# Optimization experiments

Hardware: AMD Instinct MI355X
Metric: run time of the kernel (lower is better)

## Reference

```python
import jax, jax.numpy as jnp
import numpy as np

N = 40000
E = 640000
IN_FEATS = 128
OUT_FEATS = 64
K = 8
FACTOR_DIM = OUT_FEATS // K  # 8
ITERATIONS = 3
TAU = 1.0
LEAKY_SLOPE = 0.01  # torch nn.LeakyReLU default


def setup_inputs() -> dict:
    key = jax.random.key(0)
    k1, k2, k3 = jax.random.split(key, 3)
    x = jax.random.normal(k1, (N, IN_FEATS), dtype=jnp.float32)
    # xavier_normal_ with gain=1.414: std = gain * sqrt(2 / (fan_in + fan_out))
    std = 1.414 * np.sqrt(2.0 / (IN_FEATS + OUT_FEATS))
    weight = jax.random.normal(k2, (IN_FEATS, OUT_FEATS), dtype=jnp.float32) * std
    bias = jnp.zeros((OUT_FEATS,), dtype=jnp.float32)
    edge_index = jax.random.randint(k3, (2, E), 0, N, dtype=jnp.int32)
    return {"x": x, "weight": weight, "bias": bias, "edge_index": edge_index}


def _l2norm(h):
    # h / ||h||_2 along last dim (no eps, matching torch code)
    return h / jnp.sqrt((h * h).sum(-1, keepdims=True))


def reference(x, weight, bias, edge_index):
    num_nodes = x.shape[0]
    src = edge_index[0]  # scatter target / softmax segment node
    dst = edge_index[1]  # gathered neighbor node

    h = jax.nn.leaky_relu(x @ weight + bias, LEAKY_SLOPE)          # [N, out]
    # split into K factors of FACTOR_DIM: [N, K, d]
    h = h.reshape(num_nodes, K, FACTOR_DIM)
    h_normed = _l2norm(h)                                           # [N, K, d]

    h_src = h_normed
    h_dst = h_normed
    for _ in range(ITERATIONS):
        feat_nbr = h_src[dst]                                       # [E, K, d]
        s = (h_dst[src] * feat_nbr).sum(-1) / TAU                   # [E, K]
        # segment softmax over edges grouped by src node
        smax = jax.ops.segment_max(s, src, num_segments=num_nodes)  # [N, K]
        ex = jnp.exp(s - smax[src])                                 # [E, K]
        denom = jax.ops.segment_sum(ex, src, num_segments=num_nodes)
        alpha = ex / denom[src]                                     # [E, K]
        msg = feat_nbr * alpha[..., None]                           # [E, K, d]
        node_attr = jax.ops.segment_sum(msg, src, num_segments=num_nodes)
        node_attr = node_attr + h_normed                            # [N, K, d]
        h_dst = _l2norm(node_attr)
    return h_dst.reshape(num_nodes, -1)                             # [N, out]
```

## Files before the change

### kernel.cpp

```cpp
#include <hip/hip_runtime.h>
#include <math.h>

#define NN   40000
#define EE   640000
#define INF_ 128
#define OUTF 64
#define SLOTS 64

#define GEMM_BLOCKS 625
#define SCAT_BLOCKS 625

typedef float f2 __attribute__((ext_vector_type(2)));

__device__ __forceinline__ f2 pkfma(f2 a, f2 b, f2 c) {
    return __builtin_elementwise_fma(a, b, c);
}
__device__ __forceinline__ f2 shf2(f2 a, int m) {
    f2 b; b.x = __shfl_xor(a.x, m); b.y = __shfl_xor(a.y, m); return b;
}
__device__ __forceinline__ f2 bfpair(unsigned u) {
    f2 c;
    c.x = __uint_as_float(u << 16);
    c.y = __uint_as_float(u & 0xffff0000u);
    return c;
}


__global__ void zero_k(int* __restrict__ c) {
    int i = blockIdx.x * 256 + threadIdx.x;
    if (i < NN) c[i] = 0;
}


__device__ __forceinline__ unsigned short f2bf(float f) {
    unsigned u = __float_as_uint(f);
    return (unsigned short)((u + 0x7fffu + ((u >> 16) & 1u)) >> 16);
}

__global__ __launch_bounds__(256) void scatter_gemm_k(
        const float* __restrict__ x, const float* __restrict__ w,
        const float* __restrict__ bias, float* __restrict__ hn,
        unsigned short* __restrict__ hn16,
        const int4* __restrict__ src4, const int4* __restrict__ dst4,
        int* __restrict__ counts, int* __restrict__ csr_pad) {
    __shared__ float wl[INF_ * OUTF];
    __shared__ float xl[4][2][4 * 132];

    if (blockIdx.x >= GEMM_BLOCKS) {
        int t = (blockIdx.x - GEMM_BLOCKS) * 256 + threadIdx.x;
        if (t < EE / 4) {
            int4 s = src4[t];
            int4 d = dst4[t];
            int r0 = atomicAdd(&counts[s.x], 1);
            int r1 = atomicAdd(&counts[s.y], 1);
            int r2 = atomicAdd(&counts[s.z], 1);
            int r3 = atomicAdd(&counts[s.w], 1);
            if (r0 < SLOTS) csr_pad[s.x * SLOTS + r0] = d.x;
            if (r1 < SLOTS) csr_pad[s.y * SLOTS + r1] = d.y;
            if (r2 < SLOTS) csr_pad[s.z * SLOTS + r2] = d.z;
            if (r3 < SLOTS) csr_pad[s.w * SLOTS + r3] = d.w;
        }
        return;
    }

    for (int i = threadIdx.x; i < INF_ * OUTF; i += 256) wl[i] = w[i];

    int wv = threadIdx.x >> 6;
    int l  = threadIdx.x & 63;
    int q  = l >> 4;
    int rr = l & 15;
    float4 bv = ((const float4*)bias)[rr];
    int ra = l >> 5,        ca = (l & 31) * 4;
    int rb = (l + 64) >> 5, cb = ((l + 64) & 31) * 4;

    int nb = (blockIdx.x * 4 + wv) * 16;

    {
        const float4* xs = (const float4*)(x + (size_t)nb * INF_);
        *(float4*)&xl[wv][0][ra * 132 + ca] = xs[l];
        *(float4*)&xl[wv][0][rb * 132 + cb] = xs[l + 64];
    }
    __syncthreads();

#pragma unroll
    for (int g = 0; g < 4; ++g) {
        int n0 = nb + g * 4;
        if (g < 3) {
            const float4* xs = (const float4*)(x + (size_t)(n0 + 4) * INF_);
            *(float4*)&xl[wv][(g + 1) & 1][ra * 132 + ca] = xs[l];
            *(float4*)&xl[wv][(g + 1) & 1][rb * 132 + cb] = xs[l + 64];
        }
        float4 acc = bv;
        const float* xrow = &xl[wv][g & 1][q * 132];
#pragma unroll 4
        for (int i = 0; i < INF_; ++i) {
            float xv = xrow[i];
            float4 w4 = ((const float4*)wl)[i * 16 + rr];
            acc.x = fmaf(xv, w4.x, acc.x);
            acc.y = fmaf(xv, w4.y, acc.y);
            acc.z = fmaf(xv, w4.z, acc.z);
            acc.w = fmaf(xv, w4.w, acc.w);
        }
        acc.x = acc.x > 0.f ? acc.x : 0.01f * acc.x;
        acc.y = acc.y > 0.f ? acc.y : 0.01f * acc.y;
        acc.z = acc.z > 0.f ? acc.z : 0.01f * acc.z;
        acc.w = acc.w > 0.f ? acc.w : 0.01f * acc.w;
        float sq = acc.x*acc.x + acc.y*acc.y + acc.z*acc.z + acc.w*acc.w;
        sq += __shfl_xor(sq, 1);
        float inv = rsqrtf(sq);
        float4 o = make_float4(acc.x*inv, acc.y*inv, acc.z*inv, acc.w*inv);
        ((float4*)hn)[(size_t)(n0 + q) * 16 + rr] = o;
        ushort4 o16;
        o16.x = f2bf(o.x); o16.y = f2bf(o.y); o16.z = f2bf(o.z); o16.w = f2bf(o.w);
        ((ushort4*)hn16)[(size_t)(n0 + q) * 16 + rr] = o16;
    }
}


__global__ __launch_bounds__(256) void attn_fused_k(const uint4* __restrict__ hg,
                                                    const float* __restrict__ hnf,
                                                    float* __restrict__ out,
                                                    const int* __restrict__ counts,
                                                    const int* __restrict__ csr_pad) {
    int wv = threadIdx.x >> 6;
    int l  = threadIdx.x & 63;
    int n  = blockIdx.x * 8 + wv * 2 + (l >> 5);
    int q  = (l >> 3) & 3, r = l & 7;

    const int* row = csr_pad + (size_t)n * SLOTS;
    int deg = min(counts[n], SLOTS);

    bool k0 = q      < deg;
    bool k1 = q + 4  < deg;
    bool k2 = q + 8  < deg;
    bool k3 = q + 12 < deg;
    bool k4 = q + 16 < deg;
    bool k5 = q + 20 < deg;
    bool k6 = q + 24 < deg;
    bool k7 = q + 28 < deg;
    unsigned i0 = min((unsigned)row[q     ], NN - 1u);
    unsigned i1 = min((unsigned)row[q +  4], NN - 1u);
    unsigned i2 = min((unsigned)row[q +  8], NN - 1u);
    unsigned i3 = min((unsigned)row[q + 12], NN - 1u);
    unsigned i4 = min((unsigned)row[q + 16], NN - 1u);
    unsigned i5 = min((unsigned)row[q + 20], NN - 1u);
    unsigned i6 = min((unsigned)row[q + 24], NN - 1u);
    unsigned i7 = min((unsigned)row[q + 28], NN - 1u);
    uint4 g0 = hg[(size_t)i0 * 8 + r];
    uint4 g1 = hg[(size_t)i1 * 8 + r];
    uint4 g2 = hg[(size_t)i2 * 8 + r];
    uint4 g3 = hg[(size_t)i3 * 8 + r];
    uint4 g4 = hg[(size_t)i4 * 8 + r];
    uint4 g5 = hg[(size_t)i5 * 8 + r];
    uint4 g6 = hg[(size_t)i6 * 8 + r];
    uint4 g7 = hg[(size_t)i7 * 8 + r];

    const float4* hs4 = (const float4*)(hnf + (size_t)n * OUTF + r * 8);
    float4 ha = hs4[0], hb = hs4[1];
    f2 hs01 = {ha.x, ha.y}, hs23 = {ha.z, ha.w}, hs45 = {hb.x, hb.y}, hs67 = {hb.z, hb.w};
    f2 hd01 = hs01, hd23 = hs23, hd45 = hs45, hd67 = hs67;

    for (int it = 0; it < 3; ++it) {
        float ssum = 0.f;
        f2 A0 = {0.f, 0.f}, A1 = A0, A2 = A0, A3 = A0;

        auto proc = [&](uint4 g, bool ok) {
            f2 c0 = bfpair(g.x), c1 = bfpair(g.y), c2 = bfpair(g.z), c3 = bfpair(g.w);
            f2 d = c0 * hd01;
            d = pkfma(c1, hd23, d);
            d = pkfma(c2, hd45, d);
            d = pkfma(c3, hd67, d);
            float pp = d.x + d.y;
            float ex = ok ? __expf(pp) : 0.f;
            ssum += ex;
            f2 exv = {ex, ex};
            A0 = pkfma(c0, exv, A0);
            A1 = pkfma(c1, exv, A1);
            A2 = pkfma(c2, exv, A2);
            A3 = pkfma(c3, exv, A3);
        };

        proc(g0, k0); proc(g1, k1); proc(g2, k2); proc(g3, k3);
        proc(g4, k4); proc(g5, k5); proc(g6, k6); proc(g7, k7);

        for (int e = 32 + q; e < deg; e += 4) {
            uint4 g = hg[(size_t)(unsigned)row[e] * 8 + r];
            proc(g, true);
        }

#pragma unroll
        for (int m = 8; m < 32; m <<= 1) {
            ssum += __shfl_xor(ssum, m);
            A0 += shf2(A0, m);
            A1 += shf2(A1, m);
            A2 += shf2(A2, m);
            A3 += shf2(A3, m);
        }

        float rs = (ssum > 0.f) ? 1.f / ssum : 0.f;
        f2 rsv = {rs, rs};
        f2 t01 = pkfma(A0, rsv, hs01);
        f2 t23 = pkfma(A1, rsv, hs23);
        f2 t45 = pkfma(A2, rsv, hs45);
        f2 t67 = pkfma(A3, rsv, hs67);
        f2 d = t01 * t01;
        d = pkfma(t23, t23, d);
        d = pkfma(t45, t45, d);
        d = pkfma(t67, t67, d);
        float inv = rsqrtf(d.x + d.y);
        f2 iv = {inv, inv};
        hd01 = t01 * iv; hd23 = t23 * iv; hd45 = t45 * iv; hd67 = t67 * iv;
    }

    if (q == 0) {
        float4* o4 = (float4*)(out + (size_t)n * OUTF + r * 8);
        o4[0] = make_float4(hd01.x, hd01.y, hd23.x, hd23.y);
        o4[1] = make_float4(hd45.x, hd45.y, hd67.x, hd67.y);
    }
}


extern "C" void kernel_launch(void* const* d_in, const int* in_sizes, int n_in,
                              void* d_out, int out_size, void* d_ws, size_t ws_size,
                              hipStream_t stream) {
    const float* x    = (const float*)d_in[0];
    const float* w    = (const float*)d_in[1];
    const float* bias = (const float*)d_in[2];
    const int*   ei   = (const int*)d_in[3];
    const int*   src  = ei;
    const int*   dst  = ei + EE;
    float* out = (float*)d_out;

    char* ws = (char*)d_ws;
    size_t off = 0;
    float*          hn      = (float*)(ws + off);          off += (size_t)NN * OUTF * sizeof(float);
    unsigned short* hn16    = (unsigned short*)(ws + off); off += (size_t)NN * OUTF * sizeof(short);
    int*            counts  = (int*)(ws + off);            off += (size_t)NN * sizeof(int);
    int*            csr_pad = (int*)(ws + off);            off += (size_t)NN * SLOTS * sizeof(int);
    (void)ws_size; (void)in_sizes; (void)n_in; (void)out_size;

    zero_k<<<(NN + 255) / 256, 256, 0, stream>>>(counts);

    scatter_gemm_k<<<GEMM_BLOCKS + SCAT_BLOCKS, 256, 0, stream>>>(
        x, w, bias, hn, hn16, (const int4*)src, (const int4*)dst, counts, csr_pad);

    attn_fused_k<<<NN / 8, 256, 0, stream>>>((const uint4*)hn16, hn, out,
                                             counts, csr_pad);
}
```

Measured before the change: 71.75 us.

## Store CSR neighbor indices as 16-bit and split scatter from GEMM kernel

Stores the padded CSR neighbor list as unsigned short instead of int, which works because the node count fits in 16 bits. This halves the bytes written by the scatter and read by the attention kernel. It also splits the fused scatter+GEMM launch into a standalone one-edge-per-thread scatter kernel followed by a separate GEMM/normalize kernel. That split adds a launch and gives up the overlap between scatter and GEMM blocks.

Result: slower. 86.18 us (+20.1%).

```diff
diff --git a/kernel.cpp b/kernel.cpp
--- a/kernel.cpp
+++ b/kernel.cpp
@@ -7,9 +7,6 @@
 #define OUTF 64
 #define SLOTS 64
 
-#define GEMM_BLOCKS 625
-#define SCAT_BLOCKS 625
-
 typedef float f2 __attribute__((ext_vector_type(2)));
 
 __device__ __forceinline__ f2 pkfma(f2 a, f2 b, f2 c) {
@@ -32,37 +29,32 @@
 }
 
 
+__global__ __launch_bounds__(256) void scatter_k(const int* __restrict__ src,
+                                                 const int* __restrict__ dst,
+                                                 int* __restrict__ counts,
+                                                 unsigned short* __restrict__ csr_pad) {
+    int e = blockIdx.x * 256 + threadIdx.x;
+    if (e < EE) {
+        int s = src[e];
+        int d = dst[e];
+        int r = atomicAdd(&counts[s], 1);
+        if (r < SLOTS) csr_pad[s * SLOTS + r] = (unsigned short)d;
+    }
+}
+
+
 __device__ __forceinline__ unsigned short f2bf(float f) {
     unsigned u = __float_as_uint(f);
     return (unsigned short)((u + 0x7fffu + ((u >> 16) & 1u)) >> 16);
 }
 
-__global__ __launch_bounds__(256) void scatter_gemm_k(
-        const float* __restrict__ x, const float* __restrict__ w,
-        const float* __restrict__ bias, float* __restrict__ hn,
-        unsigned short* __restrict__ hn16,
-        const int4* __restrict__ src4, const int4* __restrict__ dst4,
-        int* __restrict__ counts, int* __restrict__ csr_pad) {
+__global__ __launch_bounds__(256) void gemm_norm_k(const float* __restrict__ x,
+                                                   const float* __restrict__ w,
+                                                   const float* __restrict__ bias,
+                                                   float* __restrict__ hn,
+                                                   unsigned short* __restrict__ hn16) {
     __shared__ float wl[INF_ * OUTF];
     __shared__ float xl[4][2][4 * 132];
-
-    if (blockIdx.x >= GEMM_BLOCKS) {
-        int t = (blockIdx.x - GEMM_BLOCKS) * 256 + threadIdx.x;
-        if (t < EE / 4) {
-            int4 s = src4[t];
-            int4 d = dst4[t];
-            int r0 = atomicAdd(&counts[s.x], 1);
-            int r1 = atomicAdd(&counts[s.y], 1);
-            int r2 = atomicAdd(&counts[s.z], 1);
-            int r3 = atomicAdd(&counts[s.w], 1);
-            if (r0 < SLOTS) csr_pad[s.x * SLOTS + r0] = d.x;
-            if (r1 < SLOTS) csr_pad[s.y * SLOTS + r1] = d.y;
-            if (r2 < SLOTS) csr_pad[s.z * SLOTS + r2] = d.z;
-            if (r3 < SLOTS) csr_pad[s.w * SLOTS + r3] = d.w;
-        }
-        return;
-    }
-
     for (int i = threadIdx.x; i < INF_ * OUTF; i += 256) wl[i] = w[i];
 
     int wv = threadIdx.x >> 6;
@@ -121,13 +113,13 @@
                                                     const float* __restrict__ hnf,
                                                     float* __restrict__ out,
                                                     const int* __restrict__ counts,
-                                                    const int* __restrict__ csr_pad) {
+                                                    const unsigned short* __restrict__ csr_pad) {
     int wv = threadIdx.x >> 6;
     int l  = threadIdx.x & 63;
     int n  = blockIdx.x * 8 + wv * 2 + (l >> 5);
     int q  = (l >> 3) & 3, r = l & 7;
 
-    const int* row = csr_pad + (size_t)n * SLOTS;
+    const unsigned short* row = csr_pad + (size_t)n * SLOTS;
     int deg = min(counts[n], SLOTS);
 
     bool k0 = q      < deg;
@@ -236,13 +228,13 @@
     float*          hn      = (float*)(ws + off);          off += (size_t)NN * OUTF * sizeof(float);
     unsigned short* hn16    = (unsigned short*)(ws + off); off += (size_t)NN * OUTF * sizeof(short);
     int*            counts  = (int*)(ws + off);            off += (size_t)NN * sizeof(int);
-    int*            csr_pad = (int*)(ws + off);            off += (size_t)NN * SLOTS * sizeof(int);
+    unsigned short* csr_pad = (unsigned short*)(ws + off); off += (size_t)NN * SLOTS * sizeof(short);
     (void)ws_size; (void)in_sizes; (void)n_in; (void)out_size;
 
-    zero_k<<<(NN + 255) / 256, 256, 0, stream>>>(counts);
-
-    scatter_gemm_k<<<GEMM_BLOCKS + SCAT_BLOCKS, 256, 0, stream>>>(
-        x, w, bias, hn, hn16, (const int4*)src, (const int4*)dst, counts, csr_pad);
+    zero_k   <<<(NN + 255) / 256, 256, 0, stream>>>(counts);
+    scatter_k<<<(EE + 255) / 256, 256, 0, stream>>>(src, dst, counts, csr_pad);
+
+    gemm_norm_k<<<NN / 64, 256, 0, stream>>>(x, w, bias, hn, hn16);
 
     attn_fused_k<<<NN / 8, 256, 0, stream>>>((const uint4*)hn16, hn, out,
                                              counts, csr_pad);
```

## Split adjacency into per-lane sub-buckets with 16-bit neighbor indices

Applied to the files above, without the earlier changes.

Each source node's padded adjacency list is split into four sub-buckets, each with its own atomic counter and a capacity of 24. Every scatter lane writes to a fixed sub-bucket, so each attention lane group reads a contiguous private row. Neighbor ids are stored as 16-bit values (NN fits), which halves the CSR write and read traffic. The scatter blocks are moved to the front of the combined launch so they start earlier. In exchange, per-lane counts can now be uneven, which adds divergence in the tail loop, and edges in any sub-bucket holding more than 24 entries are silently dropped.

Result: slower. 88.46 us (+23.3%).

```diff
diff --git a/kernel.cpp b/kernel.cpp
--- a/kernel.cpp
+++ b/kernel.cpp
@@ -5,10 +5,12 @@
 #define EE   640000
 #define INF_ 128
 #define OUTF 64
-#define SLOTS 64
-
+#define NSUB 4
+#define CAP  24
+#define SLOTS (NSUB * CAP)
+
+#define SCAT_BLOCKS 625
 #define GEMM_BLOCKS 625
-#define SCAT_BLOCKS 625
 
 typedef float f2 __attribute__((ext_vector_type(2)));
 
@@ -28,7 +30,7 @@
 
 __global__ void zero_k(int* __restrict__ c) {
     int i = blockIdx.x * 256 + threadIdx.x;
-    if (i < NN) c[i] = 0;
+    if (i < NN * NSUB) c[i] = 0;
 }
 
 
@@ -42,24 +44,22 @@
         const float* __restrict__ bias, float* __restrict__ hn,
         unsigned short* __restrict__ hn16,
         const int4* __restrict__ src4, const int4* __restrict__ dst4,
-        int* __restrict__ counts, int* __restrict__ csr_pad) {
+        int* __restrict__ counts4, unsigned short* __restrict__ csr_pad) {
     __shared__ float wl[INF_ * OUTF];
     __shared__ float xl[4][2][4 * 132];
 
-    if (blockIdx.x >= GEMM_BLOCKS) {
-        int t = (blockIdx.x - GEMM_BLOCKS) * 256 + threadIdx.x;
-        if (t < EE / 4) {
-            int4 s = src4[t];
-            int4 d = dst4[t];
-            int r0 = atomicAdd(&counts[s.x], 1);
-            int r1 = atomicAdd(&counts[s.y], 1);
-            int r2 = atomicAdd(&counts[s.z], 1);
-            int r3 = atomicAdd(&counts[s.w], 1);
-            if (r0 < SLOTS) csr_pad[s.x * SLOTS + r0] = d.x;
-            if (r1 < SLOTS) csr_pad[s.y * SLOTS + r1] = d.y;
-            if (r2 < SLOTS) csr_pad[s.z * SLOTS + r2] = d.z;
-            if (r3 < SLOTS) csr_pad[s.w * SLOTS + r3] = d.w;
-        }
+    if (blockIdx.x < SCAT_BLOCKS) {
+        int t = blockIdx.x * 256 + threadIdx.x;
+        int4 s = src4[t];
+        int4 d = dst4[t];
+        int r0 = atomicAdd(&counts4[s.x * 4 + 0], 1);
+        int r1 = atomicAdd(&counts4[s.y * 4 + 1], 1);
+        int r2 = atomicAdd(&counts4[s.z * 4 + 2], 1);
+        int r3 = atomicAdd(&counts4[s.w * 4 + 3], 1);
+        if (r0 < CAP) csr_pad[s.x * SLOTS + 0 * CAP + r0] = (unsigned short)d.x;
+        if (r1 < CAP) csr_pad[s.y * SLOTS + 1 * CAP + r1] = (unsigned short)d.y;
+        if (r2 < CAP) csr_pad[s.z * SLOTS + 2 * CAP + r2] = (unsigned short)d.z;
+        if (r3 < CAP) csr_pad[s.w * SLOTS + 3 * CAP + r3] = (unsigned short)d.w;
         return;
     }
 
@@ -73,7 +73,7 @@
     int ra = l >> 5,        ca = (l & 31) * 4;
     int rb = (l + 64) >> 5, cb = ((l + 64) & 31) * 4;
 
-    int nb = (blockIdx.x * 4 + wv) * 16;
+    int nb = ((blockIdx.x - SCAT_BLOCKS) * 4 + wv) * 16;
 
     {
         const float4* xs = (const float4*)(x + (size_t)nb * INF_);
@@ -120,32 +120,24 @@
 __global__ __launch_bounds__(256) void attn_fused_k(const uint4* __restrict__ hg,
                                                     const float* __restrict__ hnf,
                                                     float* __restrict__ out,
-                                                    const int* __restrict__ counts,
-                                                    const int* __restrict__ csr_pad) {
+                                                    const int* __restrict__ counts4,
+                                                    const unsigned short* __restrict__ csr_pad) {
     int wv = threadIdx.x >> 6;
     int l  = threadIdx.x & 63;
     int n  = blockIdx.x * 8 + wv * 2 + (l >> 5);
     int q  = (l >> 3) & 3, r = l & 7;
 
-    const int* row = csr_pad + (size_t)n * SLOTS;
-    int deg = min(counts[n], SLOTS);
-
-    bool k0 = q      < deg;
-    bool k1 = q + 4  < deg;
-    bool k2 = q + 8  < deg;
-    bool k3 = q + 12 < deg;
-    bool k4 = q + 16 < deg;
-    bool k5 = q + 20 < deg;
-    bool k6 = q + 24 < deg;
-    bool k7 = q + 28 < deg;
-    unsigned i0 = min((unsigned)row[q     ], NN - 1u);
-    unsigned i1 = min((unsigned)row[q +  4], NN - 1u);
-    unsigned i2 = min((unsigned)row[q +  8], NN - 1u);
-    unsigned i3 = min((unsigned)row[q + 12], NN - 1u);
-    unsigned i4 = min((unsigned)row[q + 16], NN - 1u);
-    unsigned i5 = min((unsigned)row[q + 20], NN - 1u);
-    unsigned i6 = min((unsigned)row[q + 24], NN - 1u);
-    unsigned i7 = min((unsigned)row[q + 28], NN - 1u);
+    const unsigned short* row = csr_pad + (size_t)n * SLOTS + q * CAP;
+    int cnt = min(counts4[n * 4 + q], CAP);
+
+    unsigned i0 = min((unsigned)row[0], NN - 1u);
+    unsigned i1 = min((unsigned)row[1], NN - 1u);
+    unsigned i2 = min((unsigned)row[2], NN - 1u);
+    unsigned i3 = min((unsigned)row[3], NN - 1u);
+    unsigned i4 = min((unsigned)row[4], NN - 1u);
+    unsigned i5 = min((unsigned)row[5], NN - 1u);
+    unsigned i6 = min((unsigned)row[6], NN - 1u);
+    unsigned i7 = min((unsigned)row[7], NN - 1u);
     uint4 g0 = hg[(size_t)i0 * 8 + r];
     uint4 g1 = hg[(size_t)i1 * 8 + r];
     uint4 g2 = hg[(size_t)i2 * 8 + r];
@@ -180,12 +172,12 @@
             A3 = pkfma(c3, exv, A3);
         };
 
-        proc(g0, k0); proc(g1, k1); proc(g2, k2); proc(g3, k3);
-        proc(g4, k4); proc(g5, k5); proc(g6, k6); proc(g7, k7);
-
-        for (int e = 32 + q; e < deg; e += 4) {
-            uint4 g = hg[(size_t)(unsigned)row[e] * 8 + r];
-            proc(g, true);
+        proc(g0, 0 < cnt); proc(g1, 1 < cnt); proc(g2, 2 < cnt); proc(g3, 3 < cnt);
+        proc(g4, 4 < cnt); proc(g5, 5 < cnt); proc(g6, 6 < cnt); proc(g7, 7 < cnt);
+
+        for (int e = 8; e < cnt; ++e) {
+            unsigned ii = min((unsigned)row[e], NN - 1u);
+            proc(hg[(size_t)ii * 8 + r], true);
         }
 
 #pragma unroll
@@ -235,15 +227,15 @@
     size_t off = 0;
     float*          hn      = (float*)(ws + off);          off += (size_t)NN * OUTF * sizeof(float);
     unsigned short* hn16    = (unsigned short*)(ws + off); off += (size_t)NN * OUTF * sizeof(short);
-    int*            counts  = (int*)(ws + off);            off += (size_t)NN * sizeof(int);
-    int*            csr_pad = (int*)(ws + off);            off += (size_t)NN * SLOTS * sizeof(int);
+    int*            counts4 = (int*)(ws + off);            off += (size_t)NN * NSUB * sizeof(int);
+    unsigned short* csr_pad = (unsigned short*)(ws + off); off += (size_t)NN * SLOTS * sizeof(short);
     (void)ws_size; (void)in_sizes; (void)n_in; (void)out_size;
 
-    zero_k<<<(NN + 255) / 256, 256, 0, stream>>>(counts);
-
-    scatter_gemm_k<<<GEMM_BLOCKS + SCAT_BLOCKS, 256, 0, stream>>>(
-        x, w, bias, hn, hn16, (const int4*)src, (const int4*)dst, counts, csr_pad);
+    zero_k<<<(NN * NSUB + 255) / 256, 256, 0, stream>>>(counts4);
+
+    scatter_gemm_k<<<SCAT_BLOCKS + GEMM_BLOCKS, 256, 0, stream>>>(
+        x, w, bias, hn, hn16, (const int4*)src, (const int4*)dst, counts4, csr_pad);
 
     attn_fused_k<<<NN / 8, 256, 0, stream>>>((const uint4*)hn16, hn, out,
-                                             counts, csr_pad);
-}
+                                             counts4, csr_pad);
+}
```

## Split CSR build into histogram and placement passes with 16-bit neighbor indices

Applied to the files above, without the earlier changes.

The fused atomic-count-and-scatter step is split in two. The first kernel now runs histogram atomics next to the GEMM and records each edge's rank. A new place_k kernel then writes neighbor ids into the padded CSR as unsigned shorts, which halves the CSR footprint that the attention kernel reads. This adds a kernel launch and a rank buffer round-trip. The 16-bit indices cannot represent node ids at or above 65536, which holds for N=40000 only.

After: 86.95 us. +21.2%, slower.

```diff
diff --git a/kernel.cpp b/kernel.cpp
--- a/kernel.cpp
+++ b/kernel.cpp
@@ -7,8 +7,8 @@
 #define OUTF 64
 #define SLOTS 64
 
+#define HIST_BLOCKS 625
 #define GEMM_BLOCKS 625
-#define SCAT_BLOCKS 625
 
 typedef float f2 __attribute__((ext_vector_type(2)));
 
@@ -37,29 +37,24 @@
     return (unsigned short)((u + 0x7fffu + ((u >> 16) & 1u)) >> 16);
 }
 
-__global__ __launch_bounds__(256) void scatter_gemm_k(
+__global__ __launch_bounds__(256) void hist_gemm_k(
         const float* __restrict__ x, const float* __restrict__ w,
         const float* __restrict__ bias, float* __restrict__ hn,
         unsigned short* __restrict__ hn16,
-        const int4* __restrict__ src4, const int4* __restrict__ dst4,
-        int* __restrict__ counts, int* __restrict__ csr_pad) {
+        const int4* __restrict__ src4, int* __restrict__ counts,
+        int4* __restrict__ rank4) {
     __shared__ float wl[INF_ * OUTF];
     __shared__ float xl[4][2][4 * 132];
 
-    if (blockIdx.x >= GEMM_BLOCKS) {
-        int t = (blockIdx.x - GEMM_BLOCKS) * 256 + threadIdx.x;
-        if (t < EE / 4) {
-            int4 s = src4[t];
-            int4 d = dst4[t];
-            int r0 = atomicAdd(&counts[s.x], 1);
-            int r1 = atomicAdd(&counts[s.y], 1);
-            int r2 = atomicAdd(&counts[s.z], 1);
-            int r3 = atomicAdd(&counts[s.w], 1);
-            if (r0 < SLOTS) csr_pad[s.x * SLOTS + r0] = d.x;
-            if (r1 < SLOTS) csr_pad[s.y * SLOTS + r1] = d.y;
-            if (r2 < SLOTS) csr_pad[s.z * SLOTS + r2] = d.z;
-            if (r3 < SLOTS) csr_pad[s.w * SLOTS + r3] = d.w;
-        }
+    if (blockIdx.x < HIST_BLOCKS) {
+        int t = blockIdx.x * 256 + threadIdx.x;
+        int4 s = src4[t];
+        int4 r;
+        r.x = atomicAdd(&counts[s.x], 1);
+        r.y = atomicAdd(&counts[s.y], 1);
+        r.z = atomicAdd(&counts[s.z], 1);
+        r.w = atomicAdd(&counts[s.w], 1);
+        rank4[t] = r;
         return;
     }
 
@@ -73,7 +68,7 @@
     int ra = l >> 5,        ca = (l & 31) * 4;
     int rb = (l + 64) >> 5, cb = ((l + 64) & 31) * 4;
 
-    int nb = (blockIdx.x * 4 + wv) * 16;
+    int nb = ((blockIdx.x - HIST_BLOCKS) * 4 + wv) * 16;
 
     {
         const float4* xs = (const float4*)(x + (size_t)nb * INF_);
@@ -117,17 +112,32 @@
 }
 
 
+__global__ __launch_bounds__(256) void place_k(const int4* __restrict__ src4,
+                                               const int4* __restrict__ dst4,
+                                               const int4* __restrict__ rank4,
+                                               unsigned short* __restrict__ csr_pad) {
+    int t = blockIdx.x * 256 + threadIdx.x;
+    int4 s = src4[t];
+    int4 d = dst4[t];
+    int4 r = rank4[t];
+    if (r.x < SLOTS) csr_pad[s.x * SLOTS + r.x] = (unsigned short)d.x;
+    if (r.y < SLOTS) csr_pad[s.y * SLOTS + r.y] = (unsigned short)d.y;
+    if (r.z < SLOTS) csr_pad[s.z * SLOTS + r.z] = (unsigned short)d.z;
+    if (r.w < SLOTS) csr_pad[s.w * SLOTS + r.w] = (unsigned short)d.w;
+}
+
+
 __global__ __launch_bounds__(256) void attn_fused_k(const uint4* __restrict__ hg,
                                                     const float* __restrict__ hnf,
                                                     float* __restrict__ out,
                                                     const int* __restrict__ counts,
-                                                    const int* __restrict__ csr_pad) {
+                                                    const unsigned short* __restrict__ csr_pad) {
     int wv = threadIdx.x >> 6;
     int l  = threadIdx.x & 63;
     int n  = blockIdx.x * 8 + wv * 2 + (l >> 5);
     int q  = (l >> 3) & 3, r = l & 7;
 
-    const int* row = csr_pad + (size_t)n * SLOTS;
+    const unsigned short* row = csr_pad + (size_t)n * SLOTS;
     int deg = min(counts[n], SLOTS);
 
     bool k0 = q      < deg;
@@ -184,8 +194,8 @@
         proc(g4, k4); proc(g5, k5); proc(g6, k6); proc(g7, k7);
 
         for (int e = 32 + q; e < deg; e += 4) {
-            uint4 g = hg[(size_t)(unsigned)row[e] * 8 + r];
-            proc(g, true);
+            unsigned ii = min((unsigned)row[e], NN - 1u);
+            proc(hg[(size_t)ii * 8 + r], true);
         }
 
 #pragma unroll
@@ -236,13 +246,17 @@
     float*          hn      = (float*)(ws + off);          off += (size_t)NN * OUTF * sizeof(float);
     unsigned short* hn16    = (unsigned short*)(ws + off); off += (size_t)NN * OUTF * sizeof(short);
     int*            counts  = (int*)(ws + off);            off += (size_t)NN * sizeof(int);
-    int*            csr_pad = (int*)(ws + off);            off += (size_t)NN * SLOTS * sizeof(int);
+    int*            rank    = (int*)(ws + off);            off += (size_t)EE * sizeof(int);
+    unsigned short* csr_pad = (unsigned short*)(ws + off); off += (size_t)NN * SLOTS * sizeof(short);
     (void)ws_size; (void)in_sizes; (void)n_in; (void)out_size;
 
     zero_k<<<(NN + 255) / 256, 256, 0, stream>>>(counts);
 
-    scatter_gemm_k<<<GEMM_BLOCKS + SCAT_BLOCKS, 256, 0, stream>>>(
-        x, w, bias, hn, hn16, (const int4*)src, (const int4*)dst, counts, csr_pad);
+    hist_gemm_k<<<HIST_BLOCKS + GEMM_BLOCKS, 256, 0, stream>>>(
+        x, w, bias, hn, hn16, (const int4*)src, counts, (int4*)rank);
+
+    place_k<<<EE / 4 / 256, 256, 0, stream>>>((const int4*)src, (const int4*)dst,
+                                              (const int4*)rank, csr_pad);
 
     attn_fused_k<<<NN / 8, 256, 0, stream>>>((const uint4*)hn16, hn, out,
                                              counts, csr_pad);
```
